# Kernel optimization log

Hardware: AMD Instinct MI355X
Metric: run time of the kernel (lower is better)

Reference implementation:

```python
import jax, jax.numpy as jnp
import numpy as np

C = 128        # attention channels (inner_channel)
OUT_C = 256    # bottleneck output channels (in_channel)
NEG = -10000000.0


def conv_bn_relu(x, W, scale, shift):
    """1x1 conv (no bias) + eval-mode BatchNorm folded to scale/shift + ReLU.
    x: [B, Cin, H, W], W: [Cout, Cin]."""
    y = jnp.einsum('oc,bchw->bohw', W, x)
    y = y * scale[None, :, None, None] + shift[None, :, None, None]
    return jax.nn.relu(y)


def setup_inputs() -> dict:
    key = jax.random.key(0)
    ks = jax.random.split(key, 20)
    B, H, W_, K = 4, 128, 128, 1024
    inp = {
        'query_feats': jax.random.normal(ks[0], (B, C, H, W_), jnp.float32),
        'key_feats':   jax.random.normal(ks[1], (B, C, K, 1), jnp.float32),
        'value_feats': jax.random.normal(ks[2], (B, C, K, 1), jnp.float32),
        'key_mask':    jax.random.randint(ks[3], (B, 1, K, 1), 0, 2).astype(bool),
    }
    s = 1.0 / np.sqrt(C)

    def mk(i, cin, cout):
        return (jax.random.normal(ks[i], (cout, cin), jnp.float32) * s,
                jnp.ones((cout,), jnp.float32),
                jnp.zeros((cout,), jnp.float32))

    inp['Wq1'], inp['sq1'], inp['bq1'] = mk(4, C, C)
    inp['Wq2'], inp['sq2'], inp['bq2'] = mk(5, C, C)
    inp['Wk1'], inp['sk1'], inp['bk1'] = mk(6, C, C)
    inp['Wk2'], inp['sk2'], inp['bk2'] = mk(7, C, C)
    inp['Wv'],  inp['sv'],  inp['bv']  = mk(8, C, C)
    inp['Wo'],  inp['so'],  inp['bo']  = mk(9, C, C)
    inp['Wb'],  inp['sb'],  inp['bb']  = mk(10, 2 * C, OUT_C)
    return inp


def reference(query_feats, key_feats, value_feats, key_mask,
              Wq1, sq1, bq1, Wq2, sq2, bq2,
              Wk1, sk1, bk1, Wk2, sk2, bk2,
              Wv, sv, bv, Wo, so, bo, Wb, sb, bb):
    B, _, H, W_ = query_feats.shape
    # projections (2 conv-bn-relu for q/k, 1 for v)
    q = conv_bn_relu(conv_bn_relu(query_feats, Wq1, sq1, bq1), Wq2, sq2, bq2)
    k = conv_bn_relu(conv_bn_relu(key_feats, Wk1, sk1, bk1), Wk2, sk2, bk2)
    v = conv_bn_relu(value_feats, Wv, sv, bv)

    q = q.reshape(B, C, -1).transpose(0, 2, 1)   # [B, HW, C]
    k = k.reshape(B, C, -1)                      # [B, C, K]
    v = v.reshape(B, C, -1).transpose(0, 2, 1)   # [B, K, C]

    sim = jnp.einsum('bqc,bck->bqk', q, k) * (C ** -0.5)   # [B, HW, K]
    m = key_mask.reshape(B, 1, -1).astype(sim.dtype)        # [B, 1, K]
    sim = sim * m + NEG * (1.0 - m)
    attn = jax.nn.softmax(sim, axis=-1)

    ctx = jnp.einsum('bqk,bkc->bqc', attn, v)               # [B, HW, C]
    ctx = ctx.transpose(0, 2, 1).reshape(B, C, H, W_)
    ctx = conv_bn_relu(ctx, Wo, so, bo)                     # out_project

    out = conv_bn_relu(jnp.concatenate([ctx, query_feats], axis=1), Wb, sb, bb)
    return out
```

## Files before the change

### kernel.cpp

```cpp
#include <hip/hip_runtime.h>
#include <hip/hip_bf16.h>

#define B_    4
#define C_    128
#define HW_   16384
#define K_    1024
#define SC2_  0.12751734f
#define NEGL_ (-1.4427e7f)
#define DTHR_ 8.0f

using bf16 = __hip_bfloat16;
typedef __bf16 b8v __attribute__((ext_vector_type(8)));
typedef __bf16 b4v __attribute__((ext_vector_type(4)));
typedef float  f4v __attribute__((ext_vector_type(4)));

__device__ __forceinline__ b8v ldb8(const void* p) { return *(const b8v*)p; }
__device__ __forceinline__ b4v ldb4(const void* p) { return *(const b4v*)p; }

#define XSTRIDE 272
#define KSTRIDE 272
#define VSTRIDE 136

__device__ __forceinline__ b8v ldw8(const float* wp, float sc) {
    const float4 a = *(const float4*)wp;
    const float4 c = *(const float4*)(wp + 4);
    b8v r;
    r[0] = (__bf16)(a.x * sc); r[1] = (__bf16)(a.y * sc);
    r[2] = (__bf16)(a.z * sc); r[3] = (__bf16)(a.w * sc);
    r[4] = (__bf16)(c.x * sc); r[5] = (__bf16)(c.y * sc);
    r[6] = (__bf16)(c.z * sc); r[7] = (__bf16)(c.w * sc);
    return r;
}

__global__ __launch_bounds__(256, 4) void prep_kernel(
    const float* __restrict__ query, const float* __restrict__ key, const float* __restrict__ val,
    const float* __restrict__ Wq1, const float* __restrict__ sq1,
    const float* __restrict__ Wq2, const float* __restrict__ sq2,
    const float* __restrict__ Wo,  const float* __restrict__ so,
    const float* __restrict__ Wb,  const float* __restrict__ sb,
    const float* __restrict__ Wk1, const float* __restrict__ sk1, const float* __restrict__ bk1,
    const float* __restrict__ Wk2, const float* __restrict__ sk2, const float* __restrict__ bk2,
    const float* __restrict__ Wv,  const float* __restrict__ sv_, const float* __restrict__ bv,
    bf16* __restrict__ qt, bf16* __restrict__ kbuf, bf16* __restrict__ vbuf,
    __bf16* __restrict__ Wq1p, __bf16* __restrict__ Wq2p,
    __bf16* __restrict__ Wop,  __bf16* __restrict__ Wbp)
{
    __shared__ __align__(16) char SM[34816];
    const int blk = blockIdx.x, t = threadIdx.x;
    const int pl64 = t & 63, cg = t >> 6;

    auto scatter_tp = [&](const float* src, int L, int p0, int b, char* dst) {
#pragma unroll 4
        for (int i2 = 0; i2 < 32; ++i2) {
            const int c = cg * 32 + i2;
            const float f = src[(size_t)(b * 128 + c) * L + p0 + pl64];
            *(__bf16*)(dst + pl64 * XSTRIDE + 2 * c) = (__bf16)f;
        }
    };

    if (blk < 32) {
        const int b = blk >> 3, n0 = (blk & 7) * 128;
        const int w = t >> 6, lane = t & 63;
        const int pl = lane & 15, quad = lane >> 4;
        const int ob = 32 * w;
        char* Xs = SM;
        char* Ys = SM + 17408;

        b8v W1f[2][4], W2f[2][4];
#pragma unroll
        for (int mt = 0; mt < 2; ++mt)
#pragma unroll
            for (int s = 0; s < 4; ++s) {
                const int row = ob + mt * 16 + pl;
                W1f[mt][s] = ldw8(Wk1 + row * 128 + s * 32 + quad * 8, sk1[row]);
                W2f[mt][s] = ldw8(Wk2 + row * 128 + s * 32 + quad * 8, sk2[row]);
            }

#pragma unroll
        for (int h = 0; h < 2; ++h) {
            const int p0 = n0 + h * 64;
            scatter_tp(key, K_, p0, b, Xs);
            __syncthreads();

            f4v acc[2][4];
#pragma unroll
            for (int mt = 0; mt < 2; ++mt)
#pragma unroll
                for (int nt = 0; nt < 4; ++nt) acc[mt][nt] = (f4v){0.f, 0.f, 0.f, 0.f};
#pragma unroll
            for (int s = 0; s < 4; ++s) {
                b8v Bf[4];
#pragma unroll
                for (int nt = 0; nt < 4; ++nt)
                    Bf[nt] = ldb8(Xs + (nt * 16 + pl) * XSTRIDE + s * 64 + quad * 16);
#pragma unroll
                for (int mt = 0; mt < 2; ++mt)
#pragma unroll
                    for (int nt = 0; nt < 4; ++nt)
                        acc[mt][nt] = __builtin_amdgcn_mfma_f32_16x16x32_bf16(W1f[mt][s], Bf[nt], acc[mt][nt], 0, 0, 0);
            }
#pragma unroll
            for (int mt = 0; mt < 2; ++mt) {
                const float4 s4 = *(const float4*)(bk1 + ob + mt * 16 + quad * 4);
                const float shf[4] = {s4.x, s4.y, s4.z, s4.w};
#pragma unroll
                for (int nt = 0; nt < 4; ++nt) {
                    b4v y;
#pragma unroll
                    for (int r = 0; r < 4; ++r) y[r] = (__bf16)fmaxf(acc[mt][nt][r] + shf[r], 0.f);
                    *(b4v*)(Ys + (nt * 16 + pl) * XSTRIDE + (ob + mt * 16 + quad * 4) * 2) = y;
                }
            }
            __syncthreads();

            f4v acc2[2][4];
#pragma unroll
            for (int mt = 0; mt < 2; ++mt)
#pragma unroll
                for (int nt = 0; nt < 4; ++nt) acc2[mt][nt] = (f4v){0.f, 0.f, 0.f, 0.f};
#pragma unroll
            for (int s = 0; s < 4; ++s) {
                b8v Bf[4];
#pragma unroll
                for (int nt = 0; nt < 4; ++nt)
                    Bf[nt] = ldb8(Ys + (nt * 16 + pl) * XSTRIDE + s * 64 + quad * 16);
#pragma unroll
                for (int mt = 0; mt < 2; ++mt)
#pragma unroll
                    for (int nt = 0; nt < 4; ++nt)
                        acc2[mt][nt] = __builtin_amdgcn_mfma_f32_16x16x32_bf16(W2f[mt][s], Bf[nt], acc2[mt][nt], 0, 0, 0);
            }
            bf16* kdst = kbuf + ((size_t)b * K_ + p0) * 128;
#pragma unroll
            for (int mt = 0; mt < 2; ++mt) {
                const float4 s4 = *(const float4*)(bk2 + ob + mt * 16 + quad * 4);
                const float shf[4] = {s4.x, s4.y, s4.z, s4.w};
#pragma unroll
                for (int nt = 0; nt < 4; ++nt) {
                    b4v y;
#pragma unroll
                    for (int r = 0; r < 4; ++r) y[r] = (__bf16)fmaxf(acc2[mt][nt][r] + shf[r], 0.f);
                    *(b4v*)(kdst + (size_t)(nt * 16 + pl) * 128 + ob + mt * 16 + quad * 4) = y;
                }
            }
            __syncthreads();
        }

        b8v Wvf[2][4];
#pragma unroll
        for (int mt = 0; mt < 2; ++mt)
#pragma unroll
            for (int s = 0; s < 4; ++s) {
                const int row = ob + mt * 16 + pl;
                Wvf[mt][s] = ldw8(Wv + row * 128 + s * 32 + quad * 8, sv_[row]);
            }
#pragma unroll
        for (int h = 0; h < 2; ++h) {
            const int p0 = n0 + h * 64;
            scatter_tp(val, K_, p0, b, Xs);
            __syncthreads();

            f4v acc[2][4];
#pragma unroll
            for (int mt = 0; mt < 2; ++mt)
#pragma unroll
                for (int nt = 0; nt < 4; ++nt) acc[mt][nt] = (f4v){0.f, 0.f, 0.f, 0.f};
#pragma unroll
            for (int s = 0; s < 4; ++s) {
                b8v Bf[4];
#pragma unroll
                for (int nt = 0; nt < 4; ++nt)
                    Bf[nt] = ldb8(Xs + (nt * 16 + pl) * XSTRIDE + s * 64 + quad * 16);
#pragma unroll
                for (int mt = 0; mt < 2; ++mt)
#pragma unroll
                    for (int nt = 0; nt < 4; ++nt)
                        acc[mt][nt] = __builtin_amdgcn_mfma_f32_16x16x32_bf16(Wvf[mt][s], Bf[nt], acc[mt][nt], 0, 0, 0);
            }
            bf16* vdst = vbuf + (size_t)b * 128 * K_;
#pragma unroll
            for (int mt = 0; mt < 2; ++mt) {
                const float4 s4 = *(const float4*)(bv + ob + mt * 16 + quad * 4);
                const float shf[4] = {s4.x, s4.y, s4.z, s4.w};
#pragma unroll
                for (int nt = 0; nt < 4; ++nt)
#pragma unroll
                    for (int r = 0; r < 4; ++r)
                        vdst[(size_t)(ob + mt * 16 + quad * 4 + r) * K_ + p0 + nt * 16 + pl]
                            = __float2bfloat16(fmaxf(acc[mt][nt][r] + shf[r], 0.f));
            }
            __syncthreads();
        }
    } else if (blk < 1056) {
        const int i = blk - 32;
        const int b = i >> 8, p0 = (i & 255) * 64;
        scatter_tp(query, HW_, p0, b, SM);
        __syncthreads();
        const int seg = t & 15;
#pragma unroll
        for (int g = 0; g < 4; ++g) {
            const int p = g * 16 + (t >> 4);
            const b8v v = ldb8(SM + p * XSTRIDE + seg * 16);
            *(b8v*)(qt + ((size_t)b * HW_ + p0 + p) * 128 + seg * 8) = v;
        }
    } else {
        const int idx = (blk - 1056) * 256 + t;
        if (idx < 16384)      { Wq1p[idx] = (__bf16)(Wq1[idx] * sq1[idx >> 7]); }
        else if (idx < 32768) { const int i2 = idx - 16384; Wq2p[i2] = (__bf16)(Wq2[i2] * sq2[i2 >> 7]); }
        else if (idx < 49152) { const int i2 = idx - 32768; Wop[i2]  = (__bf16)(Wo[i2]  * so[i2 >> 7]); }
        else                  { const int i2 = idx - 49152; Wbp[i2]  = (__bf16)(Wb[i2]  * sb[i2 >> 8]); }
    }
}

__global__ __launch_bounds__(512, 4) void mega_kernel(
    const bf16* __restrict__ qt, const bf16* __restrict__ kbuf, const bf16* __restrict__ vbuf,
    const int* __restrict__ mask,
    const __bf16* __restrict__ Wq1p, const float* __restrict__ bq1,
    const __bf16* __restrict__ Wq2p, const float* __restrict__ bq2,
    const __bf16* __restrict__ Wop,  const float* __restrict__ bo,
    const __bf16* __restrict__ Wbp,  const float* __restrict__ bb,
    float* __restrict__ out)
{
    __shared__ __align__(16) char S[69632];

    const int t = threadIdx.x, w = t >> 6, lane = t & 63;
    const int pl = lane & 15, quad = lane >> 4;
    const int n0 = blockIdx.x * 128;
    const int b  = blockIdx.y;
    const int ob = 16 * w;

    char*   RA  = S;
    __bf16* RAh = (__bf16*)S;
    __bf16* RBh = (__bf16*)(S + 34816);
    char* xl = RA + (t >> 4) * XSTRIDE + (t & 15) * 16;

    {
        const char* qg = (const char*)(qt + ((size_t)b * HW_ + n0) * 128) + t * 16;
#pragma unroll
        for (int i = 0; i < 4; ++i)
            *(float4*)(xl + i * 32 * XSTRIDE) = *(const float4*)(qg + i * 8192);
    }
    {
        b8v W1f[4], W2f[4];
#pragma unroll
        for (int s = 0; s < 4; ++s) {
            W1f[s] = ldb8(Wq1p + (ob + pl) * 128 + s * 32 + quad * 8);
            W2f[s] = ldb8(Wq2p + (ob + pl) * 128 + s * 32 + quad * 8);
        }
        __syncthreads();

        f4v a1[8];
#pragma unroll
        for (int nt = 0; nt < 8; ++nt) a1[nt] = (f4v){0.f, 0.f, 0.f, 0.f};
#pragma unroll
        for (int s = 0; s < 4; ++s) {
            b8v Bf[8];
#pragma unroll
            for (int nt = 0; nt < 8; ++nt)
                Bf[nt] = ldb8(RA + (nt * 16 + pl) * XSTRIDE + s * 64 + quad * 16);
#pragma unroll
            for (int nt = 0; nt < 8; ++nt)
                a1[nt] = __builtin_amdgcn_mfma_f32_16x16x32_bf16(W1f[s], Bf[nt], a1[nt], 0, 0, 0);
        }
        {
            const float4 s4 = *(const float4*)(bq1 + ob + quad * 4);
            const float shf[4] = {s4.x, s4.y, s4.z, s4.w};
#pragma unroll
            for (int nt = 0; nt < 8; ++nt) {
                b4v y;
#pragma unroll
                for (int r = 0; r < 4; ++r) y[r] = (__bf16)fmaxf(a1[nt][r] + shf[r], 0.f);
                *(b4v*)&RBh[(nt * 16 + pl) * 136 + ob + quad * 4] = y;
            }
        }
        __syncthreads();

        f4v a2[8];
#pragma unroll
        for (int nt = 0; nt < 8; ++nt) a2[nt] = (f4v){0.f, 0.f, 0.f, 0.f};
#pragma unroll
        for (int s = 0; s < 4; ++s) {
            b8v Bf[8];
#pragma unroll
            for (int nt = 0; nt < 8; ++nt)
                Bf[nt] = *(const b8v*)&RBh[(nt * 16 + pl) * 136 + s * 32 + quad * 8];
#pragma unroll
            for (int nt = 0; nt < 8; ++nt)
                a2[nt] = __builtin_amdgcn_mfma_f32_16x16x32_bf16(W2f[s], Bf[nt], a2[nt], 0, 0, 0);
        }
        {
            const float4 s4 = *(const float4*)(bq2 + ob + quad * 4);
            const float shf[4] = {s4.x, s4.y, s4.z, s4.w};
#pragma unroll
            for (int nt = 0; nt < 8; ++nt) {
                b4v y;
#pragma unroll
                for (int r = 0; r < 4; ++r) y[r] = (__bf16)fmaxf(a2[nt][r] + shf[r], 0.f);
                *(b4v*)&RAh[(nt * 16 + pl) * 136 + ob + quad * 4] = y;
            }
        }
        __syncthreads();
    }

    b8v qf[4];
#pragma unroll
    for (int s = 0; s < 4; ++s)
        qf[s] = ldb8(RA + (w * 16 + pl) * XSTRIDE + s * 64 + quad * 16);
    __syncthreads();

    float* bias = (float*)S;
    char* ktile = S + 4096;
    char* vtile = S + 34816;

    for (int i2 = t; i2 < K_; i2 += 512)
        bias[i2] = (mask[b * K_ + i2] != 0) ? 0.f : NEGL_;

    const bf16* kpt = kbuf + (size_t)b * K_ * 128;
    const bf16* vpt = vbuf + (size_t)b * 128 * K_;
    const char* kg = (const char*)kpt + t * 16;
    const char* vg = (const char*)(vpt + (size_t)(t >> 3) * K_) + (t & 7) * 16;
    char* kl = ktile + (t >> 4) * KSTRIDE + (t & 15) * 16;
    char* vl = vtile + (t >> 3) * VSTRIDE + (t & 7) * 16;

    float4 k_r0 = *(const float4*)(kg);
    float4 k_r1 = *(const float4*)(kg + 8192);
    float4 v_r0 = *(const float4*)(vg);
    float4 v_r1 = *(const float4*)(vg + 131072);

    f4v ac[8];
#pragma unroll
    for (int i = 0; i < 8; ++i) ac[i] = (f4v){0.f, 0.f, 0.f, 0.f};
    float mrun = -3.0e38f, lrun = 0.f;

#define RAW_BARRIER()                                                 \
    __builtin_amdgcn_sched_barrier(0);                                \
    asm volatile("s_waitcnt lgkmcnt(0)" ::: "memory");                \
    __builtin_amdgcn_s_barrier();                                     \
    __builtin_amdgcn_sched_barrier(0);

    for (int chunk = 0; chunk < 16; ++chunk) {
        const int k0 = chunk * 64;

        *(float4*)(kl)                = k_r0;
        *(float4*)(kl + 32 * KSTRIDE) = k_r1;
        *(float4*)(vl)                = v_r0;
        *(float4*)(vl + 64 * VSTRIDE) = v_r1;
        RAW_BARRIER()

        if (chunk < 15) {
            const char* kgn = kg + (chunk + 1) * 16384;
            const char* vgn = vg + (chunk + 1) * 128;
            k_r0 = *(const float4*)(kgn);
            k_r1 = *(const float4*)(kgn + 8192);
            v_r0 = *(const float4*)(vgn);
            v_r1 = *(const float4*)(vgn + 131072);
        }

        f4v sv[4];
        __builtin_amdgcn_s_setprio(1);
#pragma unroll
        for (int kt = 0; kt < 4; ++kt) {
            f4v a = (f4v){0.f, 0.f, 0.f, 0.f};
            const char* krow = ktile + (kt * 16 + pl) * KSTRIDE + quad * 16;
#pragma unroll
            for (int s = 0; s < 4; ++s)
                a = __builtin_amdgcn_mfma_f32_16x16x32_bf16(ldb8(krow + s * 64), qf[s], a, 0, 0, 0);
            const float4 b4 = *(const float4*)&bias[k0 + kt * 16 + quad * 4];
            const float bb4[4] = {b4.x, b4.y, b4.z, b4.w};
#pragma unroll
            for (int r = 0; r < 4; ++r) sv[kt][r] = a[r] * SC2_ + bb4[r];
        }
        __builtin_amdgcn_s_setprio(0);

        float ml = sv[0][0];
#pragma unroll
        for (int kt = 0; kt < 4; ++kt)
#pragma unroll
            for (int r = 0; r < 4; ++r) ml = fmaxf(ml, sv[kt][r]);
        ml = fmaxf(ml, __shfl_xor(ml, 16, 64));
        ml = fmaxf(ml, __shfl_xor(ml, 32, 64));

        if (__any(ml > mrun + DTHR_)) {
            const float mn = fmaxf(mrun, ml);
            const float al = exp2f(mrun - mn);
            lrun *= al; mrun = mn;
            float ar[4];
#pragma unroll
            for (int r = 0; r < 4; ++r) ar[r] = __shfl(al, quad * 4 + r, 64);
#pragma unroll
            for (int ct = 0; ct < 8; ++ct)
#pragma unroll
                for (int r = 0; r < 4; ++r) ac[ct][r] *= ar[r];
        }

        b4v pk[4];
        float rs = 0.f;
#pragma unroll
        for (int kt = 0; kt < 4; ++kt)
#pragma unroll
            for (int r = 0; r < 4; ++r) {
                const float p = exp2f(sv[kt][r] - mrun); rs += p; pk[kt][r] = (__bf16)p;
            }
        rs += __shfl_xor(rs, 16, 64); rs += __shfl_xor(rs, 32, 64);
        lrun += rs;

        const b8v A0 = __builtin_shufflevector(pk[0], pk[1], 0, 1, 2, 3, 4, 5, 6, 7);
        const b8v A1 = __builtin_shufflevector(pk[2], pk[3], 0, 1, 2, 3, 4, 5, 6, 7);
        __builtin_amdgcn_s_setprio(1);
#pragma unroll
        for (int ct = 0; ct < 8; ++ct) {
            const char* vrow = vtile + (ct * 16 + pl) * VSTRIDE + quad * 8;
            const b8v B0 = __builtin_shufflevector(ldb4(vrow),      ldb4(vrow + 32), 0, 1, 2, 3, 4, 5, 6, 7);
            const b8v B1 = __builtin_shufflevector(ldb4(vrow + 64), ldb4(vrow + 96), 0, 1, 2, 3, 4, 5, 6, 7);
            ac[ct] = __builtin_amdgcn_mfma_f32_16x16x32_bf16(A0, B0, ac[ct], 0, 0, 0);
            ac[ct] = __builtin_amdgcn_mfma_f32_16x16x32_bf16(A1, B1, ac[ct], 0, 0, 0);
        }
        __builtin_amdgcn_s_setprio(0);

        RAW_BARRIER()
    }
#undef RAW_BARRIER

    {
        float inv[4];
#pragma unroll
        for (int r = 0; r < 4; ++r) inv[r] = 1.f / __shfl(lrun, quad * 4 + r, 64);
#pragma unroll
        for (int ct = 0; ct < 8; ++ct)
#pragma unroll
            for (int r = 0; r < 4; ++r)
                RAh[(w * 16 + quad * 4 + r) * 136 + ct * 16 + pl] = (__bf16)(ac[ct][r] * inv[r]);
    }
    __syncthreads();

    b8v Wof[4];
#pragma unroll
    for (int s = 0; s < 4; ++s)
        Wof[s] = ldb8(Wop + (ob + pl) * 128 + s * 32 + quad * 8);

    const char* qg2 = (const char*)(qt + ((size_t)b * HW_ + n0) * 128) + t * 16;
    float4 q_s0 = *(const float4*)(qg2);
    float4 q_s1 = *(const float4*)(qg2 + 8192);
    float4 q_s2 = *(const float4*)(qg2 + 16384);
    float4 q_s3 = *(const float4*)(qg2 + 24576);

    {
        f4v f1[8];
#pragma unroll
        for (int nt = 0; nt < 8; ++nt) f1[nt] = (f4v){0.f, 0.f, 0.f, 0.f};
#pragma unroll
        for (int s = 0; s < 4; ++s) {
            b8v Bf[8];
#pragma unroll
            for (int nt = 0; nt < 8; ++nt)
                Bf[nt] = ldb8(RA + (nt * 16 + pl) * XSTRIDE + s * 64 + quad * 16);
#pragma unroll
            for (int nt = 0; nt < 8; ++nt)
                f1[nt] = __builtin_amdgcn_mfma_f32_16x16x32_bf16(Wof[s], Bf[nt], f1[nt], 0, 0, 0);
        }
        {
            const float4 s4 = *(const float4*)(bo + ob + quad * 4);
            const float shf[4] = {s4.x, s4.y, s4.z, s4.w};
#pragma unroll
            for (int nt = 0; nt < 8; ++nt) {
                b4v y;
#pragma unroll
                for (int r = 0; r < 4; ++r) y[r] = (__bf16)fmaxf(f1[nt][r] + shf[r], 0.f);
                *(b4v*)&RBh[(nt * 16 + pl) * 136 + ob + quad * 4] = y;
            }
        }
    }
    __syncthreads();

    *(float4*)(xl)                 = q_s0;
    *(float4*)(xl + 32 * XSTRIDE)  = q_s1;
    *(float4*)(xl + 64 * XSTRIDE)  = q_s2;
    *(float4*)(xl + 96 * XSTRIDE)  = q_s3;
    __syncthreads();

    {
        f4v f2[2][8];
#pragma unroll
        for (int mt = 0; mt < 2; ++mt)
#pragma unroll
            for (int nt = 0; nt < 8; ++nt) f2[mt][nt] = (f4v){0.f, 0.f, 0.f, 0.f};
#pragma unroll
        for (int ks = 0; ks < 8; ++ks) {
            b8v Af[2];
#pragma unroll
            for (int mt = 0; mt < 2; ++mt)
                Af[mt] = ldb8(Wbp + (size_t)(32 * w + mt * 16 + pl) * 256 + ks * 32 + quad * 8);
            b8v Bf[8];
            if (ks < 4) {
#pragma unroll
                for (int nt = 0; nt < 8; ++nt)
                    Bf[nt] = *(const b8v*)&RBh[(nt * 16 + pl) * 136 + ks * 32 + quad * 8];
            } else {
#pragma unroll
                for (int nt = 0; nt < 8; ++nt)
                    Bf[nt] = ldb8(RA + (nt * 16 + pl) * XSTRIDE + (ks - 4) * 64 + quad * 16);
            }
#pragma unroll
            for (int mt = 0; mt < 2; ++mt)
#pragma unroll
                for (int nt = 0; nt < 8; ++nt)
                    f2[mt][nt] = __builtin_amdgcn_mfma_f32_16x16x32_bf16(Af[mt], Bf[nt], f2[mt][nt], 0, 0, 0);
        }
#pragma unroll
        for (int mt = 0; mt < 2; ++mt) {
            const float4 s4 = *(const float4*)(bb + 32 * w + mt * 16 + quad * 4);
            const float shf[4] = {s4.x, s4.y, s4.z, s4.w};
#pragma unroll
            for (int nt = 0; nt < 8; ++nt)
#pragma unroll
                for (int r = 0; r < 4; ++r)
                    out[(size_t)(b * 256 + 32 * w + mt * 16 + quad * 4 + r) * HW_ + n0 + nt * 16 + pl]
                        = fmaxf(f2[mt][nt][r] + shf[r], 0.f);
        }
    }
}

extern "C" void kernel_launch(void* const* d_in, const int* in_sizes, int n_in,
                              void* d_out, int out_size, void* d_ws, size_t ws_size,
                              hipStream_t stream)
{
    const float* query = (const float*)d_in[0];
    const float* key   = (const float*)d_in[1];
    const float* val   = (const float*)d_in[2];
    const int*   mask  = (const int*)  d_in[3];
    const float* Wq1 = (const float*)d_in[4];  const float* sq1 = (const float*)d_in[5];  const float* bq1 = (const float*)d_in[6];
    const float* Wq2 = (const float*)d_in[7];  const float* sq2 = (const float*)d_in[8];  const float* bq2 = (const float*)d_in[9];
    const float* Wk1 = (const float*)d_in[10]; const float* sk1 = (const float*)d_in[11]; const float* bk1 = (const float*)d_in[12];
    const float* Wk2 = (const float*)d_in[13]; const float* sk2 = (const float*)d_in[14]; const float* bk2 = (const float*)d_in[15];
    const float* Wv  = (const float*)d_in[16]; const float* sv  = (const float*)d_in[17]; const float* bv  = (const float*)d_in[18];
    const float* Wo  = (const float*)d_in[19]; const float* so  = (const float*)d_in[20]; const float* bo  = (const float*)d_in[21];
    const float* Wb  = (const float*)d_in[22]; const float* sb  = (const float*)d_in[23]; const float* bb  = (const float*)d_in[24];

    char* ws = (char*)d_ws;
    bf16*   qt   = (bf16*)(ws);
    bf16*   kbuf = (bf16*)(ws + (16u << 20));
    bf16*   vbuf = (bf16*)(ws + (17u << 20));
    char*   wbase = ws + (18u << 20);
    __bf16* Wq1p = (__bf16*)(wbase);
    __bf16* Wq2p = (__bf16*)(wbase + (32u << 10));
    __bf16* Wop  = (__bf16*)(wbase + (64u << 10));
    __bf16* Wbp  = (__bf16*)(wbase + (96u << 10));
    float* outp = (float*)d_out;

    prep_kernel<<<1504, 256, 0, stream>>>(
        query, key, val,
        Wq1, sq1, Wq2, sq2, Wo, so, Wb, sb,
        Wk1, sk1, bk1, Wk2, sk2, bk2, Wv, sv, bv,
        qt, kbuf, vbuf, Wq1p, Wq2p, Wop, Wbp);
    mega_kernel<<<dim3(HW_ / 128, B_), 512, 0, stream>>>(
        qt, kbuf, vbuf, mask,
        Wq1p, bq1, Wq2p, bq2, Wop, bo, Wbp, bb, outp);
}
```

Before: 240.4 us.

## Fuse query transpose/bf16 conversion into mega kernel instead of prep pass

Moves the fp32-to-bf16 transpose of query features out of the prep kernel and into the main fused kernel, which now reads query directly and transposes through shared memory into its working tile. It still writes the bf16 transposed copy to qt, presumably for the later concat/bottleneck stage. This removes a separate read-then-reload of the transposed query and shrinks the prep grid. The cost is extra in-kernel shared-memory traffic and syncs, plus uncoalesced-ish strided fp32 reads inside the main kernel.

```diff
diff --git a/kernel.cpp b/kernel.cpp
--- a/kernel.cpp
+++ b/kernel.cpp
@@ -33,7 +33,7 @@
 }
 
 __global__ __launch_bounds__(256, 4) void prep_kernel(
-    const float* __restrict__ query, const float* __restrict__ key, const float* __restrict__ val,
+    const float* __restrict__ key, const float* __restrict__ val,
     const float* __restrict__ Wq1, const float* __restrict__ sq1,
     const float* __restrict__ Wq2, const float* __restrict__ sq2,
     const float* __restrict__ Wo,  const float* __restrict__ so,
@@ -41,7 +41,7 @@
     const float* __restrict__ Wk1, const float* __restrict__ sk1, const float* __restrict__ bk1,
     const float* __restrict__ Wk2, const float* __restrict__ sk2, const float* __restrict__ bk2,
     const float* __restrict__ Wv,  const float* __restrict__ sv_, const float* __restrict__ bv,
-    bf16* __restrict__ qt, bf16* __restrict__ kbuf, bf16* __restrict__ vbuf,
+    bf16* __restrict__ kbuf, bf16* __restrict__ vbuf,
     __bf16* __restrict__ Wq1p, __bf16* __restrict__ Wq2p,
     __bf16* __restrict__ Wop,  __bf16* __restrict__ Wbp)
 {
@@ -191,20 +191,8 @@
             }
             __syncthreads();
         }
-    } else if (blk < 1056) {
-        const int i = blk - 32;
-        const int b = i >> 8, p0 = (i & 255) * 64;
-        scatter_tp(query, HW_, p0, b, SM);
-        __syncthreads();
-        const int seg = t & 15;
-#pragma unroll
-        for (int g = 0; g < 4; ++g) {
-            const int p = g * 16 + (t >> 4);
-            const b8v v = ldb8(SM + p * XSTRIDE + seg * 16);
-            *(b8v*)(qt + ((size_t)b * HW_ + p0 + p) * 128 + seg * 8) = v;
-        }
     } else {
-        const int idx = (blk - 1056) * 256 + t;
+        const int idx = (blk - 32) * 256 + t;
         if (idx < 16384)      { Wq1p[idx] = (__bf16)(Wq1[idx] * sq1[idx >> 7]); }
         else if (idx < 32768) { const int i2 = idx - 16384; Wq2p[i2] = (__bf16)(Wq2[i2] * sq2[i2 >> 7]); }
         else if (idx < 49152) { const int i2 = idx - 32768; Wop[i2]  = (__bf16)(Wo[i2]  * so[i2 >> 7]); }
@@ -213,7 +201,8 @@
 }
 
 __global__ __launch_bounds__(512, 4) void mega_kernel(
-    const bf16* __restrict__ qt, const bf16* __restrict__ kbuf, const bf16* __restrict__ vbuf,
+    const float* __restrict__ query,
+    bf16* __restrict__ qt, const bf16* __restrict__ kbuf, const bf16* __restrict__ vbuf,
     const int* __restrict__ mask,
     const __bf16* __restrict__ Wq1p, const float* __restrict__ bq1,
     const __bf16* __restrict__ Wq2p, const float* __restrict__ bq2,
@@ -234,21 +223,40 @@
     __bf16* RBh = (__bf16*)(S + 34816);
     char* xl = RA + (t >> 4) * XSTRIDE + (t & 15) * 16;
 
+    b8v W1f[4], W2f[4];
+#pragma unroll
+    for (int s = 0; s < 4; ++s) {
+        W1f[s] = ldb8(Wq1p + (ob + pl) * 128 + s * 32 + quad * 8);
+        W2f[s] = ldb8(Wq2p + (ob + pl) * 128 + s * 32 + quad * 8);
+    }
+
     {
-        const char* qg = (const char*)(qt + ((size_t)b * HW_ + n0) * 128) + t * 16;
-#pragma unroll
-        for (int i = 0; i < 4; ++i)
-            *(float4*)(xl + i * 32 * XSTRIDE) = *(const float4*)(qg + i * 8192);
+        const float* qsrc = query + (size_t)b * 128 * HW_;
+        float* Tmp = (float*)(S + 34816);
+        const int pl64 = t & 63, cgq = t >> 6;
+        const int co = t & 15,  pb = t >> 4;
+#pragma unroll
+        for (int h = 0; h < 2; ++h) {
+            const int p0 = n0 + h * 64;
+#pragma unroll 4
+            for (int i = 0; i < 16; ++i) {
+                const int c = cgq * 16 + i;
+                Tmp[pl64 * 129 + c] = qsrc[(size_t)c * HW_ + p0 + pl64];
+            }
+            __syncthreads();
+#pragma unroll
+            for (int j = 0; j < 2; ++j) {
+                const int p = pb + 32 * j;
+                b8v v;
+#pragma unroll
+                for (int e = 0; e < 8; ++e) v[e] = (__bf16)Tmp[p * 129 + co * 8 + e];
+                *(b8v*)(RA + (h * 64 + p) * XSTRIDE + co * 16) = v;
+                *(b8v*)(qt + ((size_t)b * HW_ + p0 + p) * 128 + co * 8) = v;
+            }
+            __syncthreads();
+        }
     }
     {
-        b8v W1f[4], W2f[4];
-#pragma unroll
-        for (int s = 0; s < 4; ++s) {
-            W1f[s] = ldb8(Wq1p + (ob + pl) * 128 + s * 32 + quad * 8);
-            W2f[s] = ldb8(Wq2p + (ob + pl) * 128 + s * 32 + quad * 8);
-        }
-        __syncthreads();
-
         f4v a1[8];
 #pragma unroll
         for (int nt = 0; nt < 8; ++nt) a1[nt] = (f4v){0.f, 0.f, 0.f, 0.f};
@@ -547,12 +555,12 @@
     __bf16* Wbp  = (__bf16*)(wbase + (96u << 10));
     float* outp = (float*)d_out;
 
-    prep_kernel<<<1504, 256, 0, stream>>>(
-        query, key, val,
+    prep_kernel<<<480, 256, 0, stream>>>(
+        key, val,
         Wq1, sq1, Wq2, sq2, Wo, so, Wb, sb,
         Wk1, sk1, bk1, Wk2, sk2, bk2, Wv, sv, bv,
-        qt, kbuf, vbuf, Wq1p, Wq2p, Wop, Wbp);
+        kbuf, vbuf, Wq1p, Wq2p, Wop, Wbp);
     mega_kernel<<<dim3(HW_ / 128, B_), 512, 0, stream>>>(
-        qt, kbuf, vbuf, mask,
+        query, qt, kbuf, vbuf, mask,
         Wq1p, bq1, Wq2p, bq2, Wop, bo, Wbp, bb, outp);
 }
```

Result: slower. 248.1 us (+3.2%).
